# Optimization experiments

Measured on AMD Instinct MI355X. Metric: run time of the kernel, lower is better.

The kernel has to match this reference:

```python
import jax, jax.numpy as jnp
import numpy as np
import math

B, T, C, NH, NLQ, NLKV, DHR = 2, 1024, 2048, 16, 512, 512, 64
HS = C // NH


def _rope(x, cos, sin):
    # x: [B,T,H,D]; cos/sin: [T,D//2]. Rotates pairs (even,odd) like torch apply_rotary_emb.
    xr = x.reshape(x.shape[:-1] + (-1, 2))
    re, im = xr[..., 0], xr[..., 1]
    c = cos[None, :, None, :]
    s = sin[None, :, None, :]
    out = jnp.stack([re * c - im * s, re * s + im * c], axis=-1)
    return out.reshape(x.shape)


def setup_inputs() -> dict:
    key = jax.random.key(0)
    ks = jax.random.split(key, 9)
    sc = jnp.float32(0.02)
    x = jax.random.normal(ks[0], (B, T, C), jnp.float32)
    W_dq = jax.random.normal(ks[1], (NLQ, C), jnp.float32) * sc
    W_uq = jax.random.normal(ks[2], (C, NLQ), jnp.float32) * sc
    W_dkv = jax.random.normal(ks[3], (NLKV, C), jnp.float32) * sc
    W_uk = jax.random.normal(ks[4], (C, NLKV), jnp.float32) * sc
    W_uv = jax.random.normal(ks[5], (C, NLKV), jnp.float32) * sc
    W_qr = jax.random.normal(ks[6], (NH * DHR, NLQ), jnp.float32) * sc
    W_kr = jax.random.normal(ks[7], (DHR, C), jnp.float32) * sc
    W_o = jax.random.normal(ks[8], (C, C), jnp.float32) * sc
    inv = 1.0 / (10000.0 ** (np.arange(0, DHR, 2, dtype=np.float64) / DHR))
    fr = np.outer(np.arange(T), inv)
    freqs_cos = jnp.asarray(np.cos(fr), jnp.float32)
    freqs_sin = jnp.asarray(np.sin(fr), jnp.float32)
    return {"x": x, "freqs_cos": freqs_cos, "freqs_sin": freqs_sin,
            "W_dq": W_dq, "W_uq": W_uq, "W_dkv": W_dkv, "W_uk": W_uk,
            "W_uv": W_uv, "W_qr": W_qr, "W_kr": W_kr, "W_o": W_o}


def reference(x, freqs_cos, freqs_sin, W_dq, W_uq, W_dkv, W_uk, W_uv, W_qr, W_kr, W_o):
    # Training path of FullMHLA (no kv_cache, dropout=0).
    # Absorbed matrices: same memory reinterpretation as torch .view on [out,in] weights.
    k_eff = jnp.einsum('qhd,hdk->hqk', W_uq.reshape(NLQ, NH, HS), W_uk.reshape(NH, HS, NLKV))  # [nh,nlq,nlkv]
    v_eff = (W_uv.T @ W_o.T).reshape(NLKV, NH, HS)  # used as [nlkv,nh,hs]

    c_q = x @ W_dq.T            # [B,T,nlq]
    c_kv = x @ W_dkv.T          # [B,T,nlkv]

    # content scores: c_q @ k_eff @ c_kv^T
    q_abs = jnp.einsum('btq,hqk->bhtk', c_q, k_eff)          # [B,nh,T,nlkv]
    attn_c = jnp.einsum('bhtk,bsk->bhts', q_abs, c_kv)       # [B,nh,T,T]

    # decoupled RoPE scores
    c_kr = x @ W_kr.T                                         # [B,T,dhr]
    k_r = _rope(c_kr[:, :, None, :], freqs_cos, freqs_sin)[:, :, 0, :]   # [B,T,dhr]
    c_qr = (c_q @ W_qr.T).reshape(B, T, NH, DHR)
    q_r = _rope(c_qr, freqs_cos, freqs_sin)                   # [B,T,nh,dhr]
    attn_r = jnp.einsum('bthd,bsd->bhts', q_r, k_r)           # [B,nh,T,T]

    attn = (attn_c + attn_r) / math.sqrt(HS + DHR)
    mask = jnp.triu(jnp.ones((T, T), dtype=bool), k=1)
    attn = jnp.where(mask[None, None], jnp.float32(-jnp.inf), attn)
    attn = jax.nn.softmax(attn, axis=-1)

    # y = attn @ c_kv @ v_eff
    lat = jnp.einsum('bhts,bsk->bhtk', attn, c_kv)            # [B,nh,T,nlkv]
    y = jnp.einsum('bhtk,khd->bthd', lat, v_eff)              # [B,T,nh,hs]
    return y.reshape(B, T, C)
```

## Files before the change

kernel.cpp:

```cpp
#include <hip/hip_runtime.h>

#define Bv   2
#define Tv   1024
#define Cv   2048
#define NHv  16

typedef unsigned short u16;
typedef __attribute__((ext_vector_type(8))) short bf8_t;
typedef __attribute__((ext_vector_type(4))) float f4_t;
typedef __attribute__((ext_vector_type(4))) unsigned short u16x4;
typedef __attribute__((ext_vector_type(8))) unsigned short u16x8;

__device__ __forceinline__ u16 f2bf(float f) {
  union { float f; unsigned u; } v; v.f = f;
  unsigned r = v.u + 0x7fffu + ((v.u >> 16) & 1u);
  return (u16)(r >> 16);
}
__device__ __forceinline__ float bf2f(u16 b) {
  return __uint_as_float((unsigned)b << 16);
}
__device__ __forceinline__ void glds16(const u16* gp, u16* lp) {
  __builtin_amdgcn_global_load_lds(
      (const __attribute__((address_space(1))) void*)gp,
      (__attribute__((address_space(3))) void*)lp, 16, 0, 0);
}

struct Job {
  const u16* A; const u16* B; void* C;
  long sA1, sA2, sB1, sB2, sC1, sC2;
  int K, lda, ldb, ldc, Nact, zdiv, ntx, nty, out_bf;
};
struct JobPack3 { Job j[3]; int cum[4]; };

__global__ __launch_bounds__(256) void gemm_multi(JobPack3 P) {
  const int bid = blockIdx.x;
  const int ji = (bid >= P.cum[1] ? 1 : 0) + (bid >= P.cum[2] ? 1 : 0);
  const Job& J = P.j[ji];
  int local = bid - P.cum[ji];
  const int x = local % J.ntx;
  int rest = local / J.ntx;
  const int y = rest % J.nty;
  const int z = rest / J.nty;
  const int m0 = y * 128, n0 = x * 128;

  const int z1 = z / J.zdiv, z2 = z % J.zdiv;
  const u16* A = J.A + z1 * J.sA1 + z2 * J.sA2;
  const u16* B = J.B + z1 * J.sB1 + z2 * J.sB2;
  const int K = J.K, lda = J.lda, ldb = J.ldb, ldc = J.ldc, Nact = J.Nact;

  __shared__ u16 SMEM[16384];
  u16* As = SMEM;
  u16* Bs = SMEM + 8192;

  const int tid = threadIdx.x, w = tid >> 6, ln = tid & 63;
  const int my = w >> 1, mx = w & 1;
  const int g = ln >> 4, m = ln & 15;

  f4_t acc[4][4];
#pragma unroll
  for (int i = 0; i < 4; ++i)
#pragma unroll
    for (int j = 0; j < 4; ++j) acc[i][j] = (f4_t)0.f;

  for (int k0 = 0; k0 < K; k0 += 64) {
#pragma unroll
    for (int q = 0; q < 4; ++q) {
      int r = 32 * w + 8 * q + (ln >> 3);
      int c = ((ln & 7) - r) & 7;
      glds16(&A[(long)(m0 + r) * lda + k0 + c * 8], &As[(32 * w + 8 * q) * 64]);
      glds16(&B[(long)(n0 + r) * ldb + k0 + c * 8], &Bs[(32 * w + 8 * q) * 64]);
    }
    __syncthreads();
#pragma unroll
    for (int kh = 0; kh < 2; ++kh) {
      bf8_t af[4], bg[4];
#pragma unroll
      for (int mt = 0; mt < 4; ++mt) {
        int row = my * 64 + mt * 16 + m;
        af[mt] = *(const bf8_t*)&As[row * 64 + (((kh * 4 + g) + row) & 7) * 8];
      }
#pragma unroll
      for (int nt = 0; nt < 4; ++nt) {
        int row = mx * 64 + nt * 16 + m;
        bg[nt] = *(const bf8_t*)&Bs[row * 64 + (((kh * 4 + g) + row) & 7) * 8];
      }
#pragma unroll
      for (int mt = 0; mt < 4; ++mt)
#pragma unroll
        for (int nt = 0; nt < 4; ++nt)
          acc[mt][nt] = __builtin_amdgcn_mfma_f32_16x16x32_bf16(
              af[mt], bg[nt], acc[mt][nt], 0, 0, 0);
    }
    __syncthreads();
  }

  if (J.out_bf) {
    u16* Es = SMEM + w * 4096;
#pragma unroll
    for (int mt = 0; mt < 4; ++mt)
#pragma unroll
      for (int nt = 0; nt < 4; ++nt)
#pragma unroll
        for (int r = 0; r < 4; ++r) {
          int row = mt * 16 + g * 4 + r;
          int col = nt * 16 + m;
          Es[row * 64 + (((col >> 3) + row) & 7) * 8 + (col & 7)] =
              f2bf(acc[mt][nt][r]);
        }
    __syncthreads();
    u16* C = (u16*)J.C + z1 * J.sC1 + z2 * J.sC2;
    const long rowbase = (long)(m0 + my * 64 + ln) * ldc + n0 + mx * 64;
#pragma unroll
    for (int c = 0; c < 8; ++c) {
      if (n0 + mx * 64 + c * 8 < Nact) {
        u16x8 v = *(const u16x8*)&Es[ln * 64 + ((c + ln) & 7) * 8];
        *(u16x8*)&C[rowbase + c * 8] = v;
      }
    }
  } else {
    float* C = (float*)J.C + z1 * J.sC1 + z2 * J.sC2;
#pragma unroll
    for (int mt = 0; mt < 4; ++mt)
#pragma unroll
      for (int nt = 0; nt < 4; ++nt)
#pragma unroll
        for (int r = 0; r < 4; ++r) {
          int row = m0 + my * 64 + mt * 16 + g * 4 + r;
          int col = n0 + mx * 64 + nt * 16 + m;
          if (col < Nact) C[(long)row * ldc + col] = acc[mt][nt][r];
        }
  }
}

__global__ __launch_bounds__(256) void gemm_db(JobPack3 P) {
  const int bid = blockIdx.x;
  const int ji = (bid >= P.cum[1] ? 1 : 0) + (bid >= P.cum[2] ? 1 : 0);
  const Job& J = P.j[ji];
  int local = bid - P.cum[ji];
  const int x = local % J.ntx;
  int rest = local / J.ntx;
  const int y = rest % J.nty;
  const int z = rest / J.nty;
  const int m0 = y * 128, n0 = x * 128;

  const int z1 = z / J.zdiv, z2 = z % J.zdiv;
  const u16* A = J.A + z1 * J.sA1 + z2 * J.sA2;
  const u16* B = J.B + z1 * J.sB1 + z2 * J.sB2;
  const int K = J.K, lda = J.lda, ldb = J.ldb, ldc = J.ldc, Nact = J.Nact;

  __shared__ u16 SMEM[32768];

  const int tid = threadIdx.x, w = tid >> 6, ln = tid & 63;
  const int my = w >> 1, mx = w & 1;
  const int g = ln >> 4, m = ln & 15;

  const int sr = (ln >> 3);
  const int nk = K >> 6;

  f4_t acc[4][4];
#pragma unroll
  for (int i = 0; i < 4; ++i)
#pragma unroll
    for (int j = 0; j < 4; ++j) acc[i][j] = (f4_t)0.f;

  {
    u16* As = SMEM;
    u16* Bs = SMEM + 8192;
#pragma unroll
    for (int q = 0; q < 4; ++q) {
      int r = 32 * w + 8 * q + sr;
      int c = ((ln & 7) - r) & 7;
      glds16(&A[(long)(m0 + r) * lda + c * 8], &As[(32 * w + 8 * q) * 64]);
      glds16(&B[(long)(n0 + r) * ldb + c * 8], &Bs[(32 * w + 8 * q) * 64]);
    }
  }
  __syncthreads();

  int buf = 0;
#pragma unroll 1
  for (int t = 0; t < nk; ++t) {
    if (t + 1 < nk) {
      const int k0 = (t + 1) * 64;
      u16* As = SMEM + (buf ^ 1) * 16384;
      u16* Bs = As + 8192;
#pragma unroll
      for (int q = 0; q < 4; ++q) {
        int r = 32 * w + 8 * q + sr;
        int c = ((ln & 7) - r) & 7;
        glds16(&A[(long)(m0 + r) * lda + k0 + c * 8],
               &As[(32 * w + 8 * q) * 64]);
        glds16(&B[(long)(n0 + r) * ldb + k0 + c * 8],
               &Bs[(32 * w + 8 * q) * 64]);
      }
    }
    {
      const u16* As = SMEM + buf * 16384;
      const u16* Bs = As + 8192;
#pragma unroll
      for (int kh = 0; kh < 2; ++kh) {
        bf8_t af[4], bg[4];
#pragma unroll
        for (int mt = 0; mt < 4; ++mt) {
          int row = my * 64 + mt * 16 + m;
          af[mt] = *(const bf8_t*)&As[row * 64 + (((kh * 4 + g) + row) & 7) * 8];
        }
#pragma unroll
        for (int nt = 0; nt < 4; ++nt) {
          int row = mx * 64 + nt * 16 + m;
          bg[nt] = *(const bf8_t*)&Bs[row * 64 + (((kh * 4 + g) + row) & 7) * 8];
        }
#pragma unroll
        for (int mt = 0; mt < 4; ++mt)
#pragma unroll
          for (int nt = 0; nt < 4; ++nt)
            acc[mt][nt] = __builtin_amdgcn_mfma_f32_16x16x32_bf16(
                af[mt], bg[nt], acc[mt][nt], 0, 0, 0);
      }
    }
    __syncthreads();
    buf ^= 1;
  }

  if (J.out_bf) {
    u16* Es = SMEM + w * 4096;
#pragma unroll
    for (int mt = 0; mt < 4; ++mt)
#pragma unroll
      for (int nt = 0; nt < 4; ++nt)
#pragma unroll
        for (int r = 0; r < 4; ++r) {
          int row = mt * 16 + g * 4 + r;
          int col = nt * 16 + m;
          Es[row * 64 + (((col >> 3) + row) & 7) * 8 + (col & 7)] =
              f2bf(acc[mt][nt][r]);
        }
    __syncthreads();
    u16* C = (u16*)J.C + z1 * J.sC1 + z2 * J.sC2;
    const long rowbase = (long)(m0 + my * 64 + ln) * ldc + n0 + mx * 64;
#pragma unroll
    for (int c = 0; c < 8; ++c) {
      if (n0 + mx * 64 + c * 8 < Nact) {
        u16x8 v = *(const u16x8*)&Es[ln * 64 + ((c + ln) & 7) * 8];
        *(u16x8*)&C[rowbase + c * 8] = v;
      }
    }
  } else {
    float* C = (float*)J.C + z1 * J.sC1 + z2 * J.sC2;
#pragma unroll
    for (int mt = 0; mt < 4; ++mt)
#pragma unroll
      for (int nt = 0; nt < 4; ++nt)
#pragma unroll
        for (int r = 0; r < 4; ++r) {
          int row = m0 + my * 64 + mt * 16 + g * 4 + r;
          int col = n0 + mx * 64 + nt * 16 + m;
          if (col < Nact) C[(long)row * ldc + col] = acc[mt][nt][r];
        }
  }
}

__global__ __launch_bounds__(256, 3) void attn_part(
    const u16* __restrict__ Qcat,
    const u16* __restrict__ Kcat,
    const u16* __restrict__ ZT,
    float* __restrict__ Opart,
    float* __restrict__ ml,
    float* __restrict__ out) {
  const int x = blockIdx.x;
  const int bh = x & 31, item = x >> 5;
  const int b = bh >> 4, h = bh & 15;
  static const int qtab[40] = {2,3,4,5,6,6,7,7,8,8,9,9,10,10,10,11,11,11,
                               12,12,12,13,13,13,14,14,14,14,15,15,15,15,
                               0,1,4,5,8,9,12,13};
  static const int ctab[40] = {0,0,0,0,0,1,0,1,0,1,0,1,0,1,2,0,1,2,
                               0,1,2,0,1,2,0,1,2,3,0,1,2,3,
                               0,0,1,1,2,2,3,3};
  const int qt = qtab[item], ch = ctab[item];
  const int ns = (qt >> 1) + 1;
  const int s0t = 2 * ch, s1t = min(2 * ch + 2, ns);
  const bool full = (ch == 0) && (qt <= 3);

  __shared__ u16 As[4096];
  __shared__ u16 Bs[8192];
  __shared__ u16 Ps[8192];

  const int tid = threadIdx.x, w = tid >> 6, ln = tid & 63;
  const int g = ln >> 4, m = ln & 15;

  const u16* Qb = Qcat + (long)bh * 589824 + (long)qt * 64 * 576;
  const u16* Kb = Kcat + (long)b * 589824;
  const u16* Zb = ZT + (long)bh * 131072;

  f4_t O[8];
#pragma unroll
  for (int j = 0; j < 8; ++j) O[j] = (f4_t)0.f;
  float mrow[4], lrow[4];
#pragma unroll
  for (int r = 0; r < 4; ++r) { mrow[r] = -3e38f; lrow[r] = 0.f; }

  const float scale = 0.07216878364870322f;

  for (int st = s0t; st < s1t; ++st) {
    f4_t S[8];
#pragma unroll
    for (int j = 0; j < 8; ++j) S[j] = (f4_t)0.f;

    for (int k0 = 0; k0 < 576; k0 += 64) {
#pragma unroll
      for (int q = 0; q < 2; ++q) {
        int r = 16 * w + 8 * q + (ln >> 3);
        int c = ((ln & 7) - r) & 7;
        glds16(&Qb[(long)r * 576 + k0 + c * 8], &As[(16 * w + 8 * q) * 64]);
      }
#pragma unroll
      for (int q = 0; q < 4; ++q) {
        int r = 32 * w + 8 * q + (ln >> 3);
        int c = ((ln & 7) - r) & 7;
        glds16(&Kb[(long)(st * 128 + r) * 576 + k0 + c * 8],
               &Bs[(32 * w + 8 * q) * 64]);
      }
      __syncthreads();
#pragma unroll
      for (int kh = 0; kh < 2; ++kh) {
        int qrow = 16 * w + m;
        bf8_t af = *(const bf8_t*)&As[qrow * 64 + (((kh * 4 + g) + qrow) & 7) * 8];
#pragma unroll
        for (int nt = 0; nt < 8; ++nt) {
          int row = nt * 16 + m;
          bf8_t bb = *(const bf8_t*)&Bs[row * 64 + (((kh * 4 + g) + row) & 7) * 8];
          S[nt] = __builtin_amdgcn_mfma_f32_16x16x32_bf16(af, bb, S[nt], 0, 0, 0);
        }
      }
      __syncthreads();
    }

    const bool diag = (st == (qt >> 1));
#pragma unroll
    for (int nt = 0; nt < 8; ++nt)
#pragma unroll
      for (int r = 0; r < 4; ++r) {
        float v = S[nt][r] * scale;
        if (diag &&
            (st * 128 + nt * 16 + m) > (qt * 64 + 16 * w + g * 4 + r))
          v = -3e38f;
        S[nt][r] = v;
      }

#pragma unroll
    for (int r = 0; r < 4; ++r) {
      float mx = S[0][r];
#pragma unroll
      for (int nt = 1; nt < 8; ++nt) mx = fmaxf(mx, S[nt][r]);
#pragma unroll
      for (int o = 1; o < 16; o <<= 1) mx = fmaxf(mx, __shfl_xor(mx, o, 64));
      float mn = fmaxf(mrow[r], mx);
      float al = __expf(mrow[r] - mn);
      mrow[r] = mn;
      float rs = 0.f;
#pragma unroll
      for (int nt = 0; nt < 8; ++nt) {
        float p = __expf(S[nt][r] - mn);
        S[nt][r] = p;
        rs += p;
      }
#pragma unroll
      for (int o = 1; o < 16; o <<= 1) rs += __shfl_xor(rs, o, 64);
      lrow[r] = lrow[r] * al + rs;
#pragma unroll
      for (int nt = 0; nt < 8; ++nt) O[nt][r] *= al;
    }

#pragma unroll
    for (int nt = 0; nt < 8; ++nt) {
      int colc = nt * 2 + (m >> 3), cole = m & 7;
#pragma unroll
      for (int r = 0; r < 4; ++r) {
        int row = 16 * w + g * 4 + r;
        Ps[row * 128 + ((colc + row) & 15) * 8 + cole] = f2bf(S[nt][r]);
      }
    }

#pragma unroll
    for (int kb = 0; kb < 2; ++kb) {
      __syncthreads();
#pragma unroll
      for (int q = 0; q < 4; ++q) {
        int r = 32 * w + 8 * q + (ln >> 3);
        int c = ((ln & 7) - r) & 7;
        glds16(&Zb[(long)r * 1024 + st * 128 + kb * 64 + c * 8],
               &Bs[(32 * w + 8 * q) * 64]);
      }
      __syncthreads();
#pragma unroll
      for (int kh = 0; kh < 2; ++kh) {
        int qrow = 16 * w + m;
        int chk = kb * 8 + kh * 4 + g;
        bf8_t af = *(const bf8_t*)&Ps[qrow * 128 + ((chk + qrow) & 15) * 8];
#pragma unroll
        for (int nt = 0; nt < 8; ++nt) {
          int row = nt * 16 + m;
          bf8_t bb = *(const bf8_t*)&Bs[row * 64 + (((kh * 4 + g) + row) & 7) * 8];
          O[nt] = __builtin_amdgcn_mfma_f32_16x16x32_bf16(af, bb, O[nt], 0, 0, 0);
        }
      }
    }
    __syncthreads();
  }

  if (full) {
    float* ob = out + ((long)b * Tv + qt * 64 + 16 * w) * 2048 + h * 128;
#pragma unroll
    for (int r = 0; r < 4; ++r) {
      float inv = 1.0f / lrow[r];
#pragma unroll
      for (int nt = 0; nt < 8; ++nt)
        ob[(long)(g * 4 + r) * 2048 + nt * 16 + m] = O[nt][r] * inv;
    }
  } else {
    float* Ob = Opart + (long)x * 8192;
#pragma unroll
    for (int r = 0; r < 4; ++r) {
      int row = 16 * w + g * 4 + r;
#pragma unroll
      for (int nt = 0; nt < 8; ++nt)
        Ob[(long)row * 128 + nt * 16 + m] = O[nt][r];
      if (m == 0) {
        ml[(long)x * 128 + row] = mrow[r];
        ml[(long)x * 128 + 64 + row] = lrow[r];
      }
    }
  }
}

__global__ __launch_bounds__(256) void attn_merge(
    const float* __restrict__ Opart, const float* __restrict__ ml,
    float* __restrict__ out) {
  const int i = blockIdx.x;
  const int rg = i & 3;
  const int combo = i >> 2;
  const int bh = combo & 31, qt = 4 + (combo >> 5);
  const int b = bh >> 4, h = bh & 15;
  static const int NCH[16] = {1,1,1,1,2,2,2,2,3,3,3,3,4,4,4,4};
  static const int ITEM[64] = {
      32,0,0,0,  33,0,0,0,  0,0,0,0,   1,0,0,0,
      2,34,0,0,  3,35,0,0,  4,5,0,0,   6,7,0,0,
      8,9,36,0,  10,11,37,0, 12,13,14,0, 15,16,17,0,
      18,19,20,38, 21,22,23,39, 24,25,26,27, 28,29,30,31};
  const int nch = NCH[qt];
  const int r = threadIdx.x >> 5, c4 = threadIdx.x & 31;
  float* ob = out + ((long)b * Tv + qt * 64 + rg * 16) * 2048 + h * 128;
#pragma unroll
  for (int rr = 0; rr < 2; ++rr) {
    const int lrow = r + rr * 8;
    const int row = rg * 16 + lrow;
    float M = -3e38f, mi[4], li[4];
    for (int k = 0; k < nch; ++k) {
      long p = (long)ITEM[qt * 4 + k] * 32 + bh;
      mi[k] = ml[p * 128 + row];
      li[k] = ml[p * 128 + 64 + row];
      M = fmaxf(M, mi[k]);
    }
    float L = 0.f;
    float ax = 0.f, ay = 0.f, az = 0.f, aw = 0.f;
    for (int k = 0; k < nch; ++k) {
      long p = (long)ITEM[qt * 4 + k] * 32 + bh;
      float e = __expf(mi[k] - M);
      L += li[k] * e;
      float4 v = *(const float4*)&Opart[p * 8192 + (long)row * 128 + c4 * 4];
      ax += v.x * e; ay += v.y * e; az += v.z * e; aw += v.w * e;
    }
    const float inv = 1.0f / L;
    float4 o4 = {ax * inv, ay * inv, az * inv, aw * inv};
    *(float4*)&ob[(long)lrow * 2048 + c4 * 4] = o4;
  }
}

struct CastArgs {
  const float* src[6];
  u16* dst[6];
  long cum[7];
  const float* wkr;
  u16* w3;
};
__global__ void cast_all(CastArgs a, long total4) {
  long i = (long)blockIdx.x * 256 + threadIdx.x;
  if (i < total4) {
    int seg = 0;
    while (i >= a.cum[seg + 1]) ++seg;
    long j = i - a.cum[seg];
    float4 vv = ((const float4*)a.src[seg])[j];
    u16x4 o;
    o[0] = f2bf(vv.x); o[1] = f2bf(vv.y); o[2] = f2bf(vv.z); o[3] = f2bf(vv.w);
    ((u16x4*)a.dst[seg])[j] = o;
  } else {
    long j = i - total4;
    u16x4* W4 = (u16x4*)a.w3;
    if (j < 32768) {
      float4 vv = ((const float4*)a.wkr)[j];
      u16x4 o;
      o[0] = f2bf(vv.x); o[1] = f2bf(vv.y); o[2] = f2bf(vv.z); o[3] = f2bf(vv.w);
      W4[557056 + j] = o;
    } else if (j < 65536) {
      W4[262144 + (j - 32768)] = (u16x4)0;
    } else {
      W4[589824 + (j - 65536)] = (u16x4)0;
    }
  }
}

struct TcArgs { const float* s[3]; u16* d[3]; };
__global__ __launch_bounds__(256) void tcastg(TcArgs a) {
  const int bid = blockIdx.x;
  const int job = bid >> 10, t = bid & 1023;
  const float* in = a.s[job];
  u16* out = a.d[job];
  const int R = (job == 2) ? 512 : 2048;
  const int C = (job == 2) ? 2048 : 512;
  const int xt = (job == 2) ? 64 : 16;
  const int x = t % xt, y = t / xt;
  __shared__ u16 sm[32][33];
  const int c0 = x * 32, r0 = y * 32;
  const int tx = threadIdx.x & 31, ty = threadIdx.x >> 5;
  for (int i = ty; i < 32; i += 8)
    sm[i][tx] = f2bf(in[(long)(r0 + i) * C + c0 + tx]);
  __syncthreads();
  for (int i = ty; i < 32; i += 8)
    out[(long)(c0 + i) * R + r0 + tx] = sm[tx][i];
}

__global__ void rope_fused(u16* __restrict__ Kcat, const u16* __restrict__ cqr,
                           u16* __restrict__ Qcat,
                           const float* __restrict__ cosf,
                           const float* __restrict__ sinf) {
  int idx = blockIdx.x * 256 + threadIdx.x;
  if (idx < 65536) {
    int i = idx & 31, t = (idx >> 5) & 1023, b = idx >> 15;
    float c = cosf[t * 32 + i], s = sinf[t * 32 + i];
    u16* p = Kcat + ((long)(b * Tv + t) * 576 + 512 + 2 * i);
    float re = bf2f(p[0]), im = bf2f(p[1]);
    p[0] = f2bf(re * c - im * s);
    p[1] = f2bf(re * s + im * c);
  } else {
    int j = idx - 65536;
    int i = j & 31, h = (j >> 5) & 15, t = (j >> 9) & 1023, b = j >> 19;
    float c = cosf[t * 32 + i], s = sinf[t * 32 + i];
    const u16* src = cqr + ((long)(b * Tv + t) * 1024 + h * 64 + 2 * i);
    float re = bf2f(src[0]), im = bf2f(src[1]);
    u16* dst = Qcat + (((long)(b * NHv + h) * Tv + t) * 576 + 512 + 2 * i);
    dst[0] = f2bf(re * c - im * s);
    dst[1] = f2bf(re * s + im * c);
  }
}

__global__ void vred(const float* __restrict__ P, u16* __restrict__ veffT) {
  int i = blockIdx.x * 256 + threadIdx.x;
  float4 v0 = ((const float4*)P)[i];
  float4 v1 = ((const float4*)P)[262144 + i];
  float4 v2 = ((const float4*)P)[524288 + i];
  float4 v3 = ((const float4*)P)[786432 + i];
  u16x4 o;
  o[0] = f2bf(v0.x + v1.x + v2.x + v3.x);
  o[1] = f2bf(v0.y + v1.y + v2.y + v3.y);
  o[2] = f2bf(v0.z + v1.z + v2.z + v3.z);
  o[3] = f2bf(v0.w + v1.w + v2.w + v3.w);
  ((u16x4*)veffT)[i] = o;
}

extern "C" void kernel_launch(void* const* d_in, const int* in_sizes, int n_in,
                              void* d_out, int out_size, void* d_ws,
                              size_t ws_size, hipStream_t stream) {
  const float* x    = (const float*)d_in[0];
  const float* fcos = (const float*)d_in[1];
  const float* fsin = (const float*)d_in[2];
  const float* Wdq  = (const float*)d_in[3];
  const float* Wuq  = (const float*)d_in[4];
  const float* Wdkv = (const float*)d_in[5];
  const float* Wuk  = (const float*)d_in[6];
  const float* Wuv  = (const float*)d_in[7];
  const float* Wqr  = (const float*)d_in[8];
  const float* Wkr  = (const float*)d_in[9];
  const float* Wo   = (const float*)d_in[10];
  float* out = (float*)d_out;

  u16* ws = (u16*)d_ws;
  u16* cq     = ws;
  u16* Kcat   = cq + 1179648;
  u16* veffT  = Kcat + 1179648;
  u16* Qcat   = veffT + 1048576;
  u16* W3     = Qcat + 18874368;
  u16* x_bf   = W3 + 2490368;
  u16* Wqr_bf = x_bf + 4194304;
  u16* WuqT   = Wqr_bf + 524288;
  u16* Wo_bf  = WuqT + 1048576;
  u16* WukT   = Wo_bf + 4194304;
  u16* WuvT   = WukT + 1048576;
  u16* cqr    = WuvT + 1048576;
  u16* qup    = cqr + 2097152;
  u16* ZTbuf  = qup + 4194304;
  float* Vprt  = (float*)(ZTbuf + 4194304);
  float* Opart = Vprt + 4194304;
  float* mlbuf = Opart + 10485760;

  {
    CastArgs a;
    a.src[0] = x;    a.dst[0] = x_bf;
    a.src[1] = Wdq;  a.dst[1] = W3;
    a.src[2] = Wdkv; a.dst[2] = W3 + 576 * 2048;
    a.src[3] = Wqr;  a.dst[3] = Wqr_bf;
    a.src[4] = Wo;   a.dst[4] = Wo_bf;
    a.src[5] = Wo;   a.dst[5] = Wo_bf;
    a.cum[0] = 0;        a.cum[1] = 1048576; a.cum[2] = 1310720;
    a.cum[3] = 1572864;  a.cum[4] = 1703936; a.cum[5] = 2752512;
    a.cum[6] = 2752512;
    a.wkr = Wkr; a.w3 = W3;
    cast_all<<<11136, 256, 0, stream>>>(a, 2752512L);
  }
  {
    TcArgs t;
    t.s[0] = Wuk; t.d[0] = WukT;
    t.s[1] = Wuv; t.d[1] = WuvT;
    t.s[2] = Wuq; t.d[2] = WuqT;
    tcastg<<<3072, 256, 0, stream>>>(t);
  }

  {
    JobPack3 P;
    P.j[0] = {x_bf, W3, cq, 0, 0, (long)576 * 2048, 0, 1179648, 0,
              2048, 2048, 2048, 576, 576, 1, 5, 16, 1};
    P.j[1] = {Wo_bf, WuvT, Vprt, 512, 0, 512, 0, 1048576, 0,
              512, 2048, 2048, 512, 512, 1, 4, 16, 0};
    P.j[2] = P.j[1];
    P.cum[0] = 0; P.cum[1] = 160; P.cum[2] = 416; P.cum[3] = 416;
    gemm_db<<<416, 256, 0, stream>>>(P);
  }
  vred<<<1024, 256, 0, stream>>>(Vprt, veffT);

  {
    JobPack3 P;
    P.j[0] = {cq, WuqT, qup, 0, 0, 0, 0, 0, 0,
              512, 576, 512, 2048, 2048, 1, 16, 16, 1};
    P.j[1] = {veffT, Kcat, ZTbuf, 0, 65536, 589824, 0, 2097152, 131072,
              512, 512, 576, 1024, 1024, 16, 8, 1, 1};
    P.j[2] = {cq, Wqr_bf, cqr, 0, 0, 0, 0, 0, 0,
              512, 576, 512, 1024, 1024, 1, 8, 16, 1};
    P.cum[0] = 0; P.cum[1] = 256; P.cum[2] = 512; P.cum[3] = 640;
    gemm_db<<<640, 256, 0, stream>>>(P);
  }

  {
    JobPack3 P;
    P.j[0] = {qup, WukT, Qcat, 2097152, 128, 0, 128, 9437184, 589824,
              128, 2048, 2048, 576, 512, 16, 4, 8, 1};
    P.j[1] = P.j[0];
    P.j[2] = P.j[0];
    P.cum[0] = 0; P.cum[1] = 1024; P.cum[2] = 1024; P.cum[3] = 1024;
    gemm_multi<<<1024, 256, 0, stream>>>(P);
  }

  rope_fused<<<4352, 256, 0, stream>>>(Kcat, cqr, Qcat, fcos, fsin);

  attn_part<<<1280, 256, 0, stream>>>(Qcat, Kcat, ZTbuf, Opart, mlbuf, out);
  attn_merge<<<1536, 256, 0, stream>>>(Opart, mlbuf, out);
}
```

Baseline: 274.9 us.

## Split-K the x projection GEMM and fuse its reduction into vred

The first projection GEMM (x times W_dq/W_dkv/W_kr) now runs as a 4-way split-K job writing fp32 partials into a reused scratch buffer, raising the block count from 160 to 640 so the grid fills more compute units. The existing V-effective reduction kernel is extended to also sum these partials, convert them to bf16 and scatter them into cq and Kcat. This trades extra fp32 partial-sum traffic and a larger reduction kernel for better GPU occupancy in the GEMM phase.

```diff
diff --git a/kernel.cpp b/kernel.cpp
--- a/kernel.cpp
+++ b/kernel.cpp
@@ -552,18 +552,40 @@
   }
 }
 
-__global__ void vred(const float* __restrict__ P, u16* __restrict__ veffT) {
-  int i = blockIdx.x * 256 + threadIdx.x;
-  float4 v0 = ((const float4*)P)[i];
-  float4 v1 = ((const float4*)P)[262144 + i];
-  float4 v2 = ((const float4*)P)[524288 + i];
-  float4 v3 = ((const float4*)P)[786432 + i];
-  u16x4 o;
-  o[0] = f2bf(v0.x + v1.x + v2.x + v3.x);
-  o[1] = f2bf(v0.y + v1.y + v2.y + v3.y);
-  o[2] = f2bf(v0.z + v1.z + v2.z + v3.z);
-  o[3] = f2bf(v0.w + v1.w + v2.w + v3.w);
-  ((u16x4*)veffT)[i] = o;
+__global__ void vred2(const float* __restrict__ Vp, u16* __restrict__ veffT,
+                      const float* __restrict__ Qp, u16* __restrict__ cq,
+                      u16* __restrict__ Kcat) {
+  long i = (long)blockIdx.x * 256 + threadIdx.x;
+  if (i < 262144) {
+    float4 v0 = ((const float4*)Vp)[i];
+    float4 v1 = ((const float4*)Vp)[262144 + i];
+    float4 v2 = ((const float4*)Vp)[524288 + i];
+    float4 v3 = ((const float4*)Vp)[786432 + i];
+    u16x4 o;
+    o[0] = f2bf(v0.x + v1.x + v2.x + v3.x);
+    o[1] = f2bf(v0.y + v1.y + v2.y + v3.y);
+    o[2] = f2bf(v0.z + v1.z + v2.z + v3.z);
+    o[3] = f2bf(v0.w + v1.w + v2.w + v3.w);
+    ((u16x4*)veffT)[i] = o;
+  } else {
+    long j = i - 262144;
+    int col4 = (int)(j % 288), row = (int)(j / 288);
+    long base = (long)row * 288 + col4;
+    const float4* P0 = (const float4*)Qp;
+    float4 v0 = P0[base];
+    float4 v1 = P0[589824 + base];
+    float4 v2 = P0[1179648 + base];
+    float4 v3 = P0[1769472 + base];
+    u16x4 o;
+    o[0] = f2bf(v0.x + v1.x + v2.x + v3.x);
+    o[1] = f2bf(v0.y + v1.y + v2.y + v3.y);
+    o[2] = f2bf(v0.z + v1.z + v2.z + v3.z);
+    o[3] = f2bf(v0.w + v1.w + v2.w + v3.w);
+    int c = col4 * 4;
+    u16* dst = (c < 576) ? (cq + (long)row * 576 + c)
+                         : (Kcat + (long)row * 576 + (c - 576));
+    *(u16x4*)dst = o;
+  }
 }
 
 extern "C" void kernel_launch(void* const* d_in, const int* in_sizes, int n_in,
@@ -600,6 +622,7 @@
   float* Vprt  = (float*)(ZTbuf + 4194304);
   float* Opart = Vprt + 4194304;
   float* mlbuf = Opart + 10485760;
+  float* Qprt  = Opart;
 
   {
     CastArgs a;
@@ -625,15 +648,16 @@
 
   {
     JobPack3 P;
-    P.j[0] = {x_bf, W3, cq, 0, 0, (long)576 * 2048, 0, 1179648, 0,
-              2048, 2048, 2048, 576, 576, 1, 5, 16, 1};
+    P.j[0] = {x_bf, W3, Qprt, 0, 512, (long)576 * 2048, 512,
+              576, (long)2048 * 1152,
+              512, 2048, 2048, 1152, 576, 4, 5, 16, 0};
     P.j[1] = {Wo_bf, WuvT, Vprt, 512, 0, 512, 0, 1048576, 0,
               512, 2048, 2048, 512, 512, 1, 4, 16, 0};
     P.j[2] = P.j[1];
-    P.cum[0] = 0; P.cum[1] = 160; P.cum[2] = 416; P.cum[3] = 416;
-    gemm_db<<<416, 256, 0, stream>>>(P);
-  }
-  vred<<<1024, 256, 0, stream>>>(Vprt, veffT);
+    P.cum[0] = 0; P.cum[1] = 640; P.cum[2] = 896; P.cum[3] = 896;
+    gemm_db<<<896, 256, 0, stream>>>(P);
+  }
+  vred2<<<3328, 256, 0, stream>>>(Vprt, veffT, Qprt, cq, Kcat);
 
   {
     JobPack3 P;
```

After: 283.8 us. 3.2% more time.
